# Performance work log

Hardware: AMD Instinct MI355X
Metric: run time of the kernel (lower is better)

Reference implementation:

```python
import jax, jax.numpy as jnp
import numpy as np

B, S, E, H = 2, 2048, 1024, 8
DH = E // H          # v head dim = 128
F = DH // 2          # q/k sub-head dim = 64


def setup_inputs() -> dict:
    key = jax.random.key(0)
    ks = jax.random.split(key, 7)
    sc = E ** -0.5
    return {
        "x": jax.random.normal(ks[0], (B, S, E), dtype=jnp.float32),
        "Wq": jax.random.normal(ks[1], (E, E), dtype=jnp.float32) * sc,
        "Wk": jax.random.normal(ks[2], (E, E), dtype=jnp.float32) * sc,
        "Wv": jax.random.normal(ks[3], (E, E), dtype=jnp.float32) * sc,
        "norm_w": jnp.ones((H, DH), dtype=jnp.float32),
        "Wo": jax.random.normal(ks[4], (E, E), dtype=jnp.float32) * sc,
        "bo": jnp.zeros((E,), dtype=jnp.float32),
        "diff_weight": jnp.float32(0.2),
    }


def reference(x, Wq, Wk, Wv, norm_w, Wo, bo, diff_weight):
    b, s, e = x.shape
    # projections (Linear with weight [out,in] -> x @ W.T)
    qs = (x @ Wq.T).reshape(b, s, H, 2, F)
    ks_ = (x @ Wk.T).reshape(b, s, H, 2, F)
    vs = (x @ Wv.T).reshape(b, s, H, DH)
    scale = F ** -0.5
    # two attention branches: [2, b, h, q, k]
    scores = jnp.einsum('bqhif,bkhif->ibhqk', qs, ks_) * scale
    atts = jax.nn.softmax(scores, axis=-1)
    att = atts[0] - diff_weight * atts[1]          # [b,h,q,k]
    o = jnp.einsum('bhqk,bkhe->bqhe', att, vs)     # [b,q,h,dh]
    # RMSNorm over the joint (heads, head_dim) dims, as in nn.RMSNorm([H, DH])
    eps = jnp.finfo(o.dtype).eps
    rms = jax.lax.rsqrt(jnp.mean(o * o, axis=(-2, -1), keepdims=True) + eps)
    normed = (o * rms * norm_w).reshape(b, s, e)
    return (normed @ Wo.T + bo) * (1.0 - diff_weight)
```

## Files before the change

kernel.cpp:

```cpp
#include <hip/hip_runtime.h>
#include <hip/hip_bf16.h>
#include <math.h>


#define SDIM 2048
#define EDIM 1024
#define HDIM 8
#define DHDIM 128

typedef unsigned short u16;
typedef __attribute__((ext_vector_type(8))) short bf16x8;
typedef __attribute__((ext_vector_type(4))) short bf16x4;
typedef __attribute__((ext_vector_type(4))) u16 u16x4;
typedef __attribute__((ext_vector_type(8))) u16 u16x8;
typedef __attribute__((ext_vector_type(4))) float f32x4;

__device__ __forceinline__ u16 bf16rne(float f) {
    unsigned int u = __float_as_uint(f);
    u += 0x7fff + ((u >> 16) & 1);
    return (u16)(u >> 16);
}

__device__ __forceinline__ void gload16(void* lds, const void* g) {
    __builtin_amdgcn_global_load_lds(
        (const __attribute__((address_space(1))) unsigned int*)g,
        (__attribute__((address_space(3))) unsigned int*)lds, 16, 0, 0);
}

constexpr int GM = 4096, GN = 1024, GK = 1024;

__global__ __launch_bounds__(256) void cast_bf16(
    const float* __restrict__ x,  const float* __restrict__ wq,
    const float* __restrict__ wk, const float* __restrict__ wv,
    const float* __restrict__ wo,
    u16* __restrict__ xb,  u16* __restrict__ wqb, u16* __restrict__ wkb,
    u16* __restrict__ wvb, u16* __restrict__ wob)
{
    int bid = blockIdx.x;
    const float* src; u16* dst; int lb;
    if (bid < 2048)      { src = x;  dst = xb;  lb = bid; }
    else if (bid < 2560) { src = wq; dst = wqb; lb = bid - 2048; }
    else if (bid < 3072) { src = wk; dst = wkb; lb = bid - 2560; }
    else if (bid < 3584) { src = wv; dst = wvb; lb = bid - 3072; }
    else                 { src = wo; dst = wob; lb = bid - 3584; }
    size_t i = ((size_t)lb * 256 + threadIdx.x) * 8;
    float4 a = *(const float4*)&src[i];
    float4 b = *(const float4*)&src[i + 4];
    u16x8 o;
    o[0] = bf16rne(a.x); o[1] = bf16rne(a.y); o[2] = bf16rne(a.z); o[3] = bf16rne(a.w);
    o[4] = bf16rne(b.x); o[5] = bf16rne(b.y); o[6] = bf16rne(b.z); o[7] = bf16rne(b.w);
    *(u16x8*)&dst[i] = o;
}

#define GBUF 8192

struct GemmCore {
    f32x4 acc[4][4];
    int m0, n0, wm, wn, ln, quad;
};

__device__ __forceinline__ void gemm_core(
    GemmCore& g, const u16* __restrict__ A, const u16* __restrict__ W,
    u16* AsBase, u16* BsBase)
{
    const int tid = threadIdx.x;
    const int lane = tid & 63;
    const int wv = tid >> 6;
    g.ln = lane & 15; g.quad = lane >> 4;
    g.wm = (wv >> 1) * 64; g.wn = (wv & 1) * 64;
    g.m0 = blockIdx.y * 128; g.n0 = blockIdx.x * 128;

#pragma unroll
    for (int i = 0; i < 4; ++i)
#pragma unroll
        for (int j = 0; j < 4; ++j)
            g.acc[i][j] = (f32x4){0.f, 0.f, 0.f, 0.f};

    const int s0 = tid, s1 = tid + 256, s2 = tid + 512, s3 = tid + 768;
    const int ar0 = s0 >> 3, ac0 = ((s0 & 7) ^ (ar0 & 7)) * 8;
    const int ar1 = s1 >> 3, ac1 = ((s1 & 7) ^ (ar1 & 7)) * 8;
    const int ar2 = s2 >> 3, ac2 = ((s2 & 7) ^ (ar2 & 7)) * 8;
    const int ar3 = s3 >> 3, ac3 = ((s3 & 7) ^ (ar3 & 7)) * 8;
    const u16* pa0 = A + (size_t)(g.m0 + ar0) * GK + ac0;
    const u16* pa1 = A + (size_t)(g.m0 + ar1) * GK + ac1;
    const u16* pa2 = A + (size_t)(g.m0 + ar2) * GK + ac2;
    const u16* pa3 = A + (size_t)(g.m0 + ar3) * GK + ac3;
    const u16* pb0 = W + (size_t)(g.n0 + ar0) * GK + ac0;
    const u16* pb1 = W + (size_t)(g.n0 + ar1) * GK + ac1;
    const u16* pb2 = W + (size_t)(g.n0 + ar2) * GK + ac2;
    const u16* pb3 = W + (size_t)(g.n0 + ar3) * GK + ac3;
    u16* la0 = AsBase + s0 * 8; u16* la1 = AsBase + s1 * 8;
    u16* la2 = AsBase + s2 * 8; u16* la3 = AsBase + s3 * 8;
    u16* lb0 = BsBase + s0 * 8; u16* lb1 = BsBase + s1 * 8;
    u16* lb2 = BsBase + s2 * 8; u16* lb3 = BsBase + s3 * 8;

    gload16(la0, pa0); gload16(la1, pa1);
    gload16(la2, pa2); gload16(la3, pa3);
    gload16(lb0, pb0); gload16(lb1, pb1);
    gload16(lb2, pb2); gload16(lb3, pb3);

    for (int k0 = 0; k0 < GK; k0 += 64) {
        const int cur = (k0 >> 6) & 1;
        __syncthreads();

        if (k0 + 64 < GK) {
            const int nb = (cur ^ 1) * GBUF;
            gload16(la0 + nb, pa0 + k0 + 64); gload16(la1 + nb, pa1 + k0 + 64);
            gload16(la2 + nb, pa2 + k0 + 64); gload16(la3 + nb, pa3 + k0 + 64);
            gload16(lb0 + nb, pb0 + k0 + 64); gload16(lb1 + nb, pb1 + k0 + 64);
            gload16(lb2 + nb, pb2 + k0 + 64); gload16(lb3 + nb, pb3 + k0 + 64);
        }

        const u16* Ac = AsBase + cur * GBUF;
        const u16* Bc = BsBase + cur * GBUF;

        bf16x8 af[4][2], bfr[4][2];
#pragma unroll
        for (int t = 0; t < 4; ++t) {
#pragma unroll
            for (int kk = 0; kk < 2; ++kk) {
                const int ra = g.wm + t * 16 + g.ln;
                const int rb = g.wn + t * 16 + g.ln;
                af[t][kk]  = *(const bf16x8*)&Ac[ra * 64 + (((kk * 4 + g.quad) ^ (ra & 7)) * 8)];
                bfr[t][kk] = *(const bf16x8*)&Bc[rb * 64 + (((kk * 4 + g.quad) ^ (rb & 7)) * 8)];
            }
        }
#pragma unroll
        for (int i = 0; i < 4; ++i)
#pragma unroll
            for (int j = 0; j < 4; ++j)
#pragma unroll
                for (int kk = 0; kk < 2; ++kk)
                    g.acc[i][j] = __builtin_amdgcn_mfma_f32_16x16x32_bf16(
                        af[i][kk], bfr[j][kk], g.acc[i][j], 0, 0, 0);
    }
}

__global__ __launch_bounds__(256) void gemm_qkv(
    const u16* __restrict__ A,
    const u16* __restrict__ W0, const u16* __restrict__ W1, const u16* __restrict__ W2,
    u16* __restrict__ Qb, u16* __restrict__ Kb, u16* __restrict__ Vtb)
{
    __shared__ u16 As[2 * GBUF];
    __shared__ u16 Bs[2 * GBUF];
    const int z = blockIdx.z;
    const u16* W = (z == 0) ? W0 : ((z == 1) ? W1 : W2);
    GemmCore g;
    gemm_core(g, A, W, As, Bs);

    if (z < 2) {
        const float scl = (z == 0) ? 0.125f * 1.44269504f : 1.0f;
        u16* C = (z == 0) ? Qb : Kb;
#pragma unroll
        for (int i = 0; i < 4; ++i) {
            int rb = g.m0 + g.wm + i * 16 + g.quad * 4;
#pragma unroll
            for (int r = 0; r < 4; ++r) {
                u16* crow = C + (size_t)(rb + r) * GN + g.n0 + g.wn + g.ln;
#pragma unroll
                for (int j = 0; j < 4; ++j)
                    crow[j * 16] = bf16rne(g.acc[i][j][r] * scl);
            }
        }
    } else {
        const int bb = g.m0 >> 11;
        const int sb = (g.m0 & 2047) + g.wm + g.quad * 4;
#pragma unroll
        for (int j = 0; j < 4; ++j) {
            int dhg = g.n0 + g.wn + j * 16 + g.ln;
            int hh = dhg >> 7, dh = dhg & 127;
            u16* vrow = Vtb + ((size_t)(bb * 8 + hh) * DHDIM + dh) * SDIM + sb;
#pragma unroll
            for (int i = 0; i < 4; ++i) {
                u16x4 pk;
#pragma unroll
                for (int r = 0; r < 4; ++r) pk[r] = bf16rne(g.acc[i][j][r]);
                *(u16x4*)&vrow[i * 16] = pk;
            }
        }
    }
}

__global__ __launch_bounds__(256) void gemm_out(
    const u16* __restrict__ A, const u16* __restrict__ W,
    float* __restrict__ C, const float* __restrict__ bias,
    const float* __restrict__ dwp)
{
    __shared__ u16 As[2 * GBUF];
    __shared__ u16 Bs[2 * GBUF];
    GemmCore g;
    gemm_core(g, A, W, As, Bs);

    const float scale = 1.0f - dwp[0];
    float bv[4];
#pragma unroll
    for (int j = 0; j < 4; ++j) bv[j] = bias[g.n0 + g.wn + j * 16 + g.ln];
#pragma unroll
    for (int i = 0; i < 4; ++i) {
        int rb = g.m0 + g.wm + i * 16 + g.quad * 4;
#pragma unroll
        for (int r = 0; r < 4; ++r) {
            float* crow = C + (size_t)(rb + r) * GN + g.n0 + g.wn + g.ln;
#pragma unroll
            for (int j = 0; j < 4; ++j)
                crow[j * 16] = (g.acc[i][j][r] + bv[j]) * scale;
        }
    }
}

#define KBUF 4096
#define VBUF 8192

__global__ __launch_bounds__(256, 2) void attn_mfma(
    const u16* __restrict__ Qb, const u16* __restrict__ Kb,
    const u16* __restrict__ Vtb,
    float* __restrict__ Oacc, float* __restrict__ Lacc)
{
    __shared__ u16 Ks[2 * KBUF];
    __shared__ u16 Vs[2 * VBUF];

    const int tid = threadIdx.x;
    const int wv   = tid >> 6;
    const int lane = tid & 63;
    const int ln = lane & 15, quad = lane >> 4;
    const int lx = ln & 7;
    const int vkey = (ln >> 1) & 3;
    const int bh = blockIdx.y, b = bh >> 3, h = bh & 7;
    const int q0 = blockIdx.x * 128 + wv * 32;
    const int BR = blockIdx.z;

    const size_t qoff = (size_t)b * SDIM * EDIM + h * DHDIM + BR * 64;
    bf16x8 aq[2][2];
#pragma unroll
    for (int qt = 0; qt < 2; ++qt) {
        const u16* qp = Qb + qoff + (size_t)(q0 + qt * 16 + ln) * EDIM + quad * 8;
        aq[qt][0] = *(const bf16x8*)(qp);
        aq[qt][1] = *(const bf16x8*)(qp + 32);
    }

    const int s0 = tid, s1 = tid + 256;
    const int kr0 = s0 >> 3, kc0 = ((s0 & 7) ^ (kr0 & 7)) * 8;
    const int kr1 = s1 >> 3, kc1 = ((s1 & 7) ^ (kr1 & 7)) * 8;
    const u16* kg0 = Kb + (size_t)(b * SDIM + kr0) * EDIM + h * DHDIM + BR * 64 + kc0;
    const u16* kg1 = Kb + (size_t)(b * SDIM + kr1) * EDIM + h * DHDIM + BR * 64 + kc1;
    const int vr0 = s0 >> 2, vc0 = ((s0 & 3) ^ ((vr0 >> 1) & 3)) * 8;
    const int vr1 = s1 >> 2, vc1 = ((s1 & 3) ^ ((vr1 >> 1) & 3)) * 8;
    const u16* vg0 = Vtb + ((size_t)bh * DHDIM + vr0) * SDIM + vc0;
    const u16* vg1 = Vtb + ((size_t)bh * DHDIM + vr1) * SDIM + vc1;
    u16* ksd0 = Ks + s0 * 8; u16* ksd1 = Ks + s1 * 8;
    u16* vsd0 = Vs + s0 * 8; u16* vsd1 = Vs + s1 * 8;

    gload16(ksd0, kg0); gload16(ksd1, kg1);
    gload16(vsd0, vg0); gload16(vsd1, vg1);
    gload16(vsd0 + 4096, vg0 + 32); gload16(vsd1 + 4096, vg1 + 32);
    kg0 += 64 * EDIM; kg1 += 64 * EDIM; vg0 += 64; vg1 += 64;

    f32x4 acc[2][8];
#pragma unroll
    for (int qt = 0; qt < 2; ++qt)
#pragma unroll
        for (int d = 0; d < 8; ++d)
            acc[qt][d] = (f32x4){0.f, 0.f, 0.f, 0.f};
    float lsum[2] = {0.f, 0.f};
    const f32x4 z4 = (f32x4){0.f, 0.f, 0.f, 0.f};

    for (int it = 0; it < 32; ++it) {
        const int cur = it & 1;
        __syncthreads();

        if (it < 31) {
            const int kb = (cur ^ 1) * KBUF, vb2 = (cur ^ 1) * VBUF;
            gload16(ksd0 + kb, kg0); gload16(ksd1 + kb, kg1);
            gload16(vsd0 + vb2, vg0); gload16(vsd1 + vb2, vg1);
            gload16(vsd0 + vb2 + 4096, vg0 + 32); gload16(vsd1 + vb2 + 4096, vg1 + 32);
            kg0 += 64 * EDIM; kg1 += 64 * EDIM; vg0 += 64; vg1 += 64;
        }

        const u16* Kc = Ks + cur * KBUF;
        const u16* Vc = Vs + cur * VBUF;

        bf16x8 kf[4][2];
#pragma unroll
        for (int t2 = 0; t2 < 4; ++t2) {
            const int rb = (t2 * 16 + ln) * 64;
            kf[t2][0] = *(const bf16x8*)&Kc[rb + ((quad ^ lx) * 8)];
            kf[t2][1] = *(const bf16x8*)&Kc[rb + (((4 + quad) ^ lx) * 8)];
        }

        f32x4 st[2][4];
#pragma unroll
        for (int t2 = 0; t2 < 4; ++t2)
#pragma unroll
            for (int qt = 0; qt < 2; ++qt) {
                f32x4 s = __builtin_amdgcn_mfma_f32_16x16x32_bf16(kf[t2][0], aq[qt][0], z4, 0, 0, 0);
                st[qt][t2] = __builtin_amdgcn_mfma_f32_16x16x32_bf16(kf[t2][1], aq[qt][1], s, 0, 0, 0);
            }

        bf16x8 vf[8][2];
#pragma unroll
        for (int dt = 0; dt < 8; ++dt) {
            const int vb = (dt * 16 + ln) * 32;
#pragma unroll
            for (int ks = 0; ks < 2; ++ks) {
                const u16* Vk = Vc + ks * 4096;
                bf16x4 vlo = *(const bf16x4*)&Vk[vb + ((((quad >> 1) + 0) ^ vkey) * 8 + (quad & 1) * 4)];
                bf16x4 vhi = *(const bf16x4*)&Vk[vb + ((((quad >> 1) + 2) ^ vkey) * 8 + (quad & 1) * 4)];
                vf[dt][ks] = __builtin_shufflevector(vlo, vhi, 0, 1, 2, 3, 4, 5, 6, 7);
            }
        }

        union { unsigned int u[4]; bf16x8 v; } ap[2][2];
#pragma unroll
        for (int qt = 0; qt < 2; ++qt)
#pragma unroll
            for (int ks = 0; ks < 2; ++ks) {
                float e0 = exp2f(st[qt][2 * ks][0]), e1 = exp2f(st[qt][2 * ks][1]);
                float e2 = exp2f(st[qt][2 * ks][2]), e3 = exp2f(st[qt][2 * ks][3]);
                float f0 = exp2f(st[qt][2 * ks + 1][0]), f1 = exp2f(st[qt][2 * ks + 1][1]);
                float f2 = exp2f(st[qt][2 * ks + 1][2]), f3 = exp2f(st[qt][2 * ks + 1][3]);
                lsum[qt] += (e0 + e1) + (e2 + e3) + (f0 + f1) + (f2 + f3);
                ap[qt][ks].u[0] = __builtin_amdgcn_perm(__float_as_uint(e1), __float_as_uint(e0), 0x07060302u);
                ap[qt][ks].u[1] = __builtin_amdgcn_perm(__float_as_uint(e3), __float_as_uint(e2), 0x07060302u);
                ap[qt][ks].u[2] = __builtin_amdgcn_perm(__float_as_uint(f1), __float_as_uint(f0), 0x07060302u);
                ap[qt][ks].u[3] = __builtin_amdgcn_perm(__float_as_uint(f3), __float_as_uint(f2), 0x07060302u);
            }

#pragma unroll
        for (int dt = 0; dt < 8; ++dt)
#pragma unroll
            for (int ks = 0; ks < 2; ++ks)
#pragma unroll
                for (int qt = 0; qt < 2; ++qt)
                    acc[qt][dt] = __builtin_amdgcn_mfma_f32_16x16x32_bf16(ap[qt][ks].v, vf[dt][ks], acc[qt][dt], 0, 0, 0);
    }

#pragma unroll
    for (int qt = 0; qt < 2; ++qt) {
#pragma unroll
        for (int r = 0; r < 4; ++r) {
            size_t row = (size_t)(b * SDIM + q0 + qt * 16 + quad * 4 + r);
            float* o = Oacc + ((row * 8 + h) * 2 + BR) * 128 + ln;
#pragma unroll
            for (int dt = 0; dt < 8; ++dt)
                o[dt * 16] = acc[qt][dt][r];
        }
    }
#pragma unroll
    for (int qt = 0; qt < 2; ++qt) {
        float l = lsum[qt];
        l += __shfl_xor(l, 16, 64); l += __shfl_xor(l, 32, 64);
        if (quad == 0)
            Lacc[(size_t)((b * 8 + h) * 2 + BR) * SDIM + q0 + qt * 16 + ln] = l;
    }
}

__global__ __launch_bounds__(256) void rms_combine(
    const float* __restrict__ Oacc, const float* __restrict__ Lacc,
    const float* __restrict__ nw, u16* __restrict__ Nb,
    const float* __restrict__ dwp)
{
    const int row = blockIdx.x;
    const int tid = threadIdx.x;
    const int h = tid >> 5, dh0 = (tid & 31) * 4;
    const int b = row >> 11, q = row & 2047;

    size_t ob = ((size_t)row * 8 + h) * 2 * 128;
    f32x4 a0 = *(const f32x4*)&Oacc[ob + dh0];
    f32x4 a1 = *(const f32x4*)&Oacc[ob + 128 + dh0];
    float l0 = Lacc[(size_t)((b * 8 + h) * 2 + 0) * SDIM + q];
    float l1 = Lacc[(size_t)((b * 8 + h) * 2 + 1) * SDIM + q];
    const float dw = dwp[0];
    float inv0 = 1.0f / l0;
    float inv1 = dw / l1;
    float o[4];
#pragma unroll
    for (int k = 0; k < 4; ++k) o[k] = a0[k] * inv0 - a1[k] * inv1;

    float ss = o[0] * o[0] + o[1] * o[1] + o[2] * o[2] + o[3] * o[3];
    ss += __shfl_xor(ss, 1,  64);
    ss += __shfl_xor(ss, 2,  64);
    ss += __shfl_xor(ss, 4,  64);
    ss += __shfl_xor(ss, 8,  64);
    ss += __shfl_xor(ss, 16, 64);
    ss += __shfl_xor(ss, 32, 64);
    __shared__ float red[4];
    if ((tid & 63) == 0) red[tid >> 6] = ss;
    __syncthreads();
    float tot = red[0] + red[1] + red[2] + red[3];
    float rms = rsqrtf(tot * (1.0f / 1024.0f) + 1.1920929e-07f);

    float4 w = *(const float4*)&nw[tid * 4];
    u16x4 pk;
    pk[0] = bf16rne(o[0] * rms * w.x);
    pk[1] = bf16rne(o[1] * rms * w.y);
    pk[2] = bf16rne(o[2] * rms * w.z);
    pk[3] = bf16rne(o[3] * rms * w.w);
    *(u16x4*)&Nb[(size_t)row * EDIM + tid * 4] = pk;
}

extern "C" void kernel_launch(void* const* d_in, const int* in_sizes, int n_in,
                              void* d_out, int out_size, void* d_ws, size_t ws_size,
                              hipStream_t stream)
{
    const float* x   = (const float*)d_in[0];
    const float* Wq  = (const float*)d_in[1];
    const float* Wk  = (const float*)d_in[2];
    const float* Wv  = (const float*)d_in[3];
    const float* nw  = (const float*)d_in[4];
    const float* Wo  = (const float*)d_in[5];
    const float* bo  = (const float*)d_in[6];
    const float* dwp = (const float*)d_in[7];
    float* out = (float*)d_out;

    float* Oacc = (float*)d_ws;
    u16*  xb   = (u16*)d_ws;
    u16*  wob  = (u16*)((char*)d_ws + 33554432);
    u16*  wqb  = wob + 1048576;
    u16*  wkb  = wqb + 1048576;
    u16*  wvb  = wkb + 1048576;
    float* Lacc = (float*)wqb;
    u16*  Qb   = wvb + 1048576;
    u16*  Kb   = Qb + 4194304;
    u16*  Vtb  = Kb + 4194304;
    u16*  Nb   = Qb;

    cast_bf16<<<4096, 256, 0, stream>>>(x, Wq, Wk, Wv, Wo,
                                        xb, wqb, wkb, wvb, wob);
    gemm_qkv<<<dim3(GN / 128, GM / 128, 3), 256, 0, stream>>>(
        xb, wqb, wkb, wvb, Qb, Kb, Vtb);
    attn_mfma<<<dim3(SDIM / 128, 2 * HDIM, 2), 256, 0, stream>>>(
        Qb, Kb, Vtb, Oacc, Lacc);
    rms_combine<<<4096, 256, 0, stream>>>(Oacc, Lacc, nw, Nb, dwp);
    gemm_out<<<dim3(GN / 128, GM / 128, 1), 256, 0, stream>>>(
        Nb, wob, out, bo, dwp);
}
```

Baseline: 222.2 us.

## Swizzle GEMM block order across XCDs and stage V transpose through LDS

Block indices in the shared GEMM core are remapped so that consecutive blocks, which are dealt round-robin across the 8 XCDs, work on contiguous tiles. This aims to improve L2 reuse per XCD. The V-projection epilogue now writes the transposed tile into padded LDS and then stores 16-byte coalesced rows to global memory, replacing scattered 8-byte stores. The cost is two extra barriers and LDS traffic in the V path. The swizzle also assumes the grid size is divisible by 8.

```diff
diff --git a/kernel.cpp b/kernel.cpp
--- a/kernel.cpp
+++ b/kernel.cpp
@@ -68,7 +68,14 @@
     const int wv = tid >> 6;
     g.ln = lane & 15; g.quad = lane >> 4;
     g.wm = (wv >> 1) * 64; g.wn = (wv & 1) * 64;
-    g.m0 = blockIdx.y * 128; g.n0 = blockIdx.x * 128;
+
+    {
+        const int bid = blockIdx.y * gridDim.x + blockIdx.x;
+        const int cpx = (gridDim.x * gridDim.y) >> 3;
+        const int swz = (bid & 7) * cpx + (bid >> 3);
+        g.m0 = (swz / gridDim.x) * 128;
+        g.n0 = (swz % gridDim.x) * 128;
+    }
 
 #pragma unroll
     for (int i = 0; i < 4; ++i)
@@ -136,17 +143,18 @@
     }
 }
 
+#define TSTR 136
+
 __global__ __launch_bounds__(256) void gemm_qkv(
     const u16* __restrict__ A,
     const u16* __restrict__ W0, const u16* __restrict__ W1, const u16* __restrict__ W2,
     u16* __restrict__ Qb, u16* __restrict__ Kb, u16* __restrict__ Vtb)
 {
-    __shared__ u16 As[2 * GBUF];
-    __shared__ u16 Bs[2 * GBUF];
+    __shared__ u16 Sh[4 * GBUF];
     const int z = blockIdx.z;
     const u16* W = (z == 0) ? W0 : ((z == 1) ? W1 : W2);
     GemmCore g;
-    gemm_core(g, A, W, As, Bs);
+    gemm_core(g, A, W, Sh, Sh + 2 * GBUF);
 
     if (z < 2) {
         const float scl = (z == 0) ? 0.125f * 1.44269504f : 1.0f;
@@ -163,20 +171,32 @@
             }
         }
     } else {
+        __syncthreads();
+        u16* Ts = Sh;
+#pragma unroll
+        for (int i = 0; i < 4; ++i)
+#pragma unroll
+            for (int j = 0; j < 4; ++j) {
+                const int nl = g.wn + j * 16 + g.ln;
+                const int ml = g.wm + i * 16 + g.quad * 4;
+                u16x4 pk;
+#pragma unroll
+                for (int r = 0; r < 4; ++r) pk[r] = bf16rne(g.acc[i][j][r]);
+                *(u16x4*)&Ts[nl * TSTR + ml] = pk;
+            }
+        __syncthreads();
+
+        const int tid = threadIdx.x;
+        const int c = tid & 15;
         const int bb = g.m0 >> 11;
-        const int sb = (g.m0 & 2047) + g.wm + g.quad * 4;
-#pragma unroll
-        for (int j = 0; j < 4; ++j) {
-            int dhg = g.n0 + g.wn + j * 16 + g.ln;
-            int hh = dhg >> 7, dh = dhg & 127;
-            u16* vrow = Vtb + ((size_t)(bb * 8 + hh) * DHDIM + dh) * SDIM + sb;
-#pragma unroll
-            for (int i = 0; i < 4; ++i) {
-                u16x4 pk;
-#pragma unroll
-                for (int r = 0; r < 4; ++r) pk[r] = bf16rne(g.acc[i][j][r]);
-                *(u16x4*)&vrow[i * 16] = pk;
-            }
+        const int sb0 = g.m0 & 2047;
+        const int hh = g.n0 >> 7;
+#pragma unroll
+        for (int s = 0; s < 8; ++s) {
+            const int rown = (tid >> 4) + s * 16;
+            u16x8 v = *(const u16x8*)&Ts[rown * TSTR + c * 8];
+            u16* vrow = Vtb + (((size_t)bb * 8 + hh) * DHDIM + rown) * SDIM + sb0;
+            *(u16x8*)&vrow[c * 8] = v;
         }
     }
 }
@@ -186,10 +206,9 @@
     float* __restrict__ C, const float* __restrict__ bias,
     const float* __restrict__ dwp)
 {
-    __shared__ u16 As[2 * GBUF];
-    __shared__ u16 Bs[2 * GBUF];
+    __shared__ u16 Sh[4 * GBUF];
     GemmCore g;
-    gemm_core(g, A, W, As, Bs);
+    gemm_core(g, A, W, Sh, Sh + 2 * GBUF);
 
     const float scale = 1.0f - dwp[0];
     float bv[4];
```

Measured after the change: 213.3 us. -4.0%, faster.
